# Kernel optimization log

Hardware: AMD Instinct MI355X
Metric: run time of the kernel (lower is better)

The kernel has to match this reference:

```python
import jax, jax.numpy as jnp
import numpy as np

N = 50000
E = 800000
IN, HID, OUT, MASK = 128, 96, 40, 64
THRESHOLD = 0.5


def _glorot(key, shape):
    fan_in, fan_out = shape[0], shape[1]
    lim = np.sqrt(6.0 / (fan_in + fan_out))
    return jax.random.uniform(key, shape, jnp.float32, -lim, lim)


def setup_inputs() -> dict:
    key = jax.random.key(0)
    ks = jax.random.split(key, 10)
    x = jax.random.normal(ks[0], (N, IN), jnp.float32)
    edge_index = jax.random.randint(ks[1], (2, E), 0, N, dtype=jnp.int64)
    W1 = _glorot(ks[2], (IN, HID)); b1 = jnp.zeros((HID,), jnp.float32)
    W2 = _glorot(ks[3], (HID, OUT)); b2 = jnp.zeros((OUT,), jnp.float32)
    Wm1 = _glorot(ks[4], (HID, MASK)); bm1 = jnp.zeros((MASK,), jnp.float32)
    Wm2 = _glorot(ks[5], (MASK, 1)); bm2 = jnp.zeros((1,), jnp.float32)
    return {"x": x, "edge_index": edge_index, "W1": W1, "b1": b1,
            "W2": W2, "b2": b2, "Wm1": Wm1, "bm1": bm1, "Wm2": Wm2, "bm2": bm2}


def _gcn_conv(x, src, dst, norm, W, b, n_nodes):
    # PyG GCNConv: linear transform first, then normalized scatter-add aggregation
    h = x @ W                                   # [N, out]
    msg = h[src] * norm[:, None]                # gather + scale, [E', out]
    agg = jax.ops.segment_sum(msg, dst, num_segments=n_nodes)
    return agg + b


def reference(x, edge_index, W1, b1, W2, b2, Wm1, bm1, Wm2, bm2):
    n = x.shape[0]
    # add self-loops (A + I)
    loop = jnp.arange(n, dtype=edge_index.dtype)
    src = jnp.concatenate([edge_index[0], loop])
    dst = jnp.concatenate([edge_index[1], loop])
    # symmetric normalization D^-1/2 (A+I) D^-1/2
    deg = jax.ops.segment_sum(jnp.ones_like(dst, dtype=x.dtype), dst, num_segments=n)
    dinv = jnp.where(deg > 0, jax.lax.rsqrt(deg), 0.0)
    norm = dinv[src] * dinv[dst]                # [E+N]

    h = jax.nn.relu(_gcn_conv(x, src, dst, norm, W1, b1, n))   # [N, HID]
    # dropout_p = 0.0 -> identity
    z = _gcn_conv(h, src, dst, norm, W2, b2, n)                # [N, OUT]
    logits = jax.nn.log_softmax(z, axis=1)

    prob = jax.nn.sigmoid((jax.nn.relu(h @ Wm1 + bm1) @ Wm2 + bm2)[:, 0])  # [N]
    hard = (prob > THRESHOLD).astype(prob.dtype)
    mask = prob + (hard - jax.lax.stop_gradient(prob))          # straight-through
    return (logits, prob, mask)
```

## Files before the change

### kernel.cpp

```cpp
#include <hip/hip_runtime.h>
#include <math.h>

#define IN_F  128
#define HID   96
#define OUT_F 40
#define MASKD 64

#define PBITS 8
#define PSIZE 256
#define CHUNK 2048


__global__ void k_pzero(int* __restrict__ part_total) {
    part_total[threadIdx.x] = 0;
}

__global__ void k_pcount(const int* __restrict__ dst, int* __restrict__ part_total, int e) {
    __shared__ int hist[256];
    hist[threadIdx.x] = 0;
    __syncthreads();
    int start = blockIdx.x * CHUNK, end = min(e, start + CHUNK);
    for (int i = start + threadIdx.x; i < end; i += 256)
        atomicAdd(&hist[dst[i] >> PBITS], 1);
    __syncthreads();
    int v = hist[threadIdx.x];
    if (v) atomicAdd(&part_total[threadIdx.x], v);
}

__global__ void k_pscan(const int* __restrict__ part_total, int* __restrict__ part_base,
                        int* __restrict__ part_cursor, int np) {
    __shared__ int tmp[256];
    int tid = threadIdx.x;
    int v = (tid < np) ? part_total[tid] : 0;
    tmp[tid] = v;
    __syncthreads();
    for (int d = 1; d < 256; d <<= 1) {
        int t = (tid >= d) ? tmp[tid - d] : 0;
        __syncthreads();
        tmp[tid] += t;
        __syncthreads();
    }
    int excl = tmp[tid] - v;
    if (tid < np) { part_base[tid] = excl; part_cursor[tid] = excl; }
    if (tid == 255) part_base[np] = tmp[255];
}

__global__ __launch_bounds__(256) void k_bin(const int* __restrict__ src,
                                             const int* __restrict__ dst,
                                             int* __restrict__ part_cursor,
                                             int2* __restrict__ ebuf, int e) {
    __shared__ int hist[256];
    __shared__ int cur[256];
    int tid = threadIdx.x;
    hist[tid] = 0;
    __syncthreads();
    int start = blockIdx.x * CHUNK, end = min(e, start + CHUNK);
    for (int i = start + tid; i < end; i += 256)
        atomicAdd(&hist[dst[i] >> PBITS], 1);
    __syncthreads();
    int hv = hist[tid];
    cur[tid] = hv ? atomicAdd(&part_cursor[tid], hv) : 0;
    __syncthreads();
    for (int i = start + tid; i < end; i += 256) {
        int d = dst[i];
        int pos = atomicAdd(&cur[d >> PBITS], 1);
        ebuf[pos] = make_int2(src[i], d);
    }
}

__global__ __launch_bounds__(256) void k_csr(const int2* __restrict__ ebuf,
                                             const int* __restrict__ part_base,
                                             int* __restrict__ deg, int* __restrict__ offs,
                                             float* __restrict__ dinv,
                                             int* __restrict__ csr, int n) {
    __shared__ int cnt[256];
    __shared__ int tmp[256];
    __shared__ int cur[256];
    int tid = threadIdx.x;
    int p = blockIdx.x;
    int ebase = part_base[p], eend = part_base[p + 1];
    cnt[tid] = 0;
    __syncthreads();
    for (int i = ebase + tid; i < eend; i += 256)
        atomicAdd(&cnt[ebuf[i].y & (PSIZE - 1)], 1);
    __syncthreads();
    int v = cnt[tid];
    tmp[tid] = v;
    __syncthreads();
    for (int d = 1; d < 256; d <<= 1) {
        int t = (tid >= d) ? tmp[tid - d] : 0;
        __syncthreads();
        tmp[tid] += t;
        __syncthreads();
    }
    int goff = ebase + (tmp[tid] - v);
    int node = p * PSIZE + tid;
    if (node < n) {
        deg[node] = v;
        offs[node] = goff;
        dinv[node] = rsqrtf((float)(v + 1));
    }
    cur[tid] = goff;
    __syncthreads();
    for (int i = ebase + tid; i < eend; i += 256) {
        int2 ed = ebuf[i];
        int pos = atomicAdd(&cur[ed.y & (PSIZE - 1)], 1);
        csr[pos] = ed.x;
    }
}

#define G1_ROWS 32
__global__ __launch_bounds__(192) void k_gemm1(const float* __restrict__ x,
                                               const float* __restrict__ W1,
                                               const float* __restrict__ dinv,
                                               float* __restrict__ hs, int n) {
    __shared__ float sW[IN_F * HID];
    __shared__ float sx[G1_ROWS * IN_F];
    int tid = threadIdx.x;
    int base = blockIdx.x * G1_ROWS;
    for (int i = tid; i < IN_F * HID / 4; i += 192)
        ((float4*)sW)[i] = ((const float4*)W1)[i];
    int nt = min(G1_ROWS, n - base);
    for (int i = tid; i < nt * (IN_F / 4); i += 192) {
        int r = i >> 5, kq = i & 31;
        ((float4*)sx)[r * 32 + kq] = ((const float4*)(x + (size_t)(base + r) * IN_F))[kq];
    }
    __syncthreads();

    int rt = tid / 24, ct = tid % 24;
    float acc[4][4] = {};
#pragma unroll 1
    for (int k0 = 0; k0 < IN_F; k0 += 4) {
        float4 xv[4], wv[4];
#pragma unroll
        for (int i = 0; i < 4; i++) xv[i] = *(const float4*)&sx[(rt * 4 + i) * IN_F + k0];
#pragma unroll
        for (int j = 0; j < 4; j++) wv[j] = *(const float4*)&sW[(k0 + j) * HID + ct * 4];
#pragma unroll
        for (int j = 0; j < 4; j++) {
            float4 w = wv[j];
#pragma unroll
            for (int i = 0; i < 4; i++) {
                float xs = (j == 0) ? xv[i].x : (j == 1) ? xv[i].y : (j == 2) ? xv[i].z : xv[i].w;
                acc[i][0] += xs * w.x;
                acc[i][1] += xs * w.y;
                acc[i][2] += xs * w.z;
                acc[i][3] += xs * w.w;
            }
        }
    }
#pragma unroll
    for (int i = 0; i < 4; i++) {
        int r = rt * 4 + i;
        if (r < nt) {
            int node = base + r;
            float dv = dinv[node];
            float4 o = {acc[i][0] * dv, acc[i][1] * dv, acc[i][2] * dv, acc[i][3] * dv};
            *(float4*)(hs + (size_t)node * HID + ct * 4) = o;
        }
    }
}

__global__ __launch_bounds__(256) void k_gather1(const int* __restrict__ offs,
                                                 const int* __restrict__ deg,
                                                 const int* __restrict__ csr,
                                                 const float* __restrict__ hs,
                                                 const float* __restrict__ dinv,
                                                 const float* __restrict__ b1,
                                                 float* __restrict__ h, int n) {
    int t = blockIdx.x * 256 + threadIdx.x;
    int node = t >> 5, cg = t & 31;
    if (node >= n || cg >= 24) return;
    int o = offs[node], cnt = deg[node];
    size_t col = (size_t)cg * 4;
    float4 acc = *(const float4*)(hs + (size_t)node * HID + col);
    int k = o, kend = o + cnt;
    for (; k + 3 < kend; k += 4) {
        int s0 = csr[k], s1 = csr[k + 1], s2 = csr[k + 2], s3 = csr[k + 3];
        const float4 v0 = *(const float4*)(hs + (size_t)s0 * HID + col);
        const float4 v1 = *(const float4*)(hs + (size_t)s1 * HID + col);
        const float4 v2 = *(const float4*)(hs + (size_t)s2 * HID + col);
        const float4 v3 = *(const float4*)(hs + (size_t)s3 * HID + col);
        acc.x += (v0.x + v1.x) + (v2.x + v3.x);
        acc.y += (v0.y + v1.y) + (v2.y + v3.y);
        acc.z += (v0.z + v1.z) + (v2.z + v3.z);
        acc.w += (v0.w + v1.w) + (v2.w + v3.w);
    }
    for (; k < kend; k++) {
        int s0 = csr[k];
        const float4 v0 = *(const float4*)(hs + (size_t)s0 * HID + col);
        acc.x += v0.x; acc.y += v0.y; acc.z += v0.z; acc.w += v0.w;
    }
    float dv = dinv[node];
    float4 bv = *(const float4*)(b1 + col);
    float4 o4 = {fmaxf(acc.x * dv + bv.x, 0.f), fmaxf(acc.y * dv + bv.y, 0.f),
                 fmaxf(acc.z * dv + bv.z, 0.f), fmaxf(acc.w * dv + bv.w, 0.f)};
    *(float4*)(h + (size_t)node * HID + col) = o4;
}

#define G2_ROWS 96
__global__ __launch_bounds__(256) void k_gemm2(const float* __restrict__ hbuf,
                                               const float* __restrict__ W2,
                                               const float* __restrict__ dinv,
                                               float* __restrict__ zs, int n) {
    __shared__ float sW[HID * OUT_F];
    __shared__ float sx[G2_ROWS * HID];
    int tid = threadIdx.x;
    int base = blockIdx.x * G2_ROWS;
    for (int i = tid; i < HID * OUT_F / 4; i += 256)
        ((float4*)sW)[i] = ((const float4*)W2)[i];
    int nt = min(G2_ROWS, n - base);
    for (int i = tid; i < nt * (HID / 4); i += 256) {
        int r = i / 24, kq = i % 24;
        ((float4*)sx)[r * 24 + kq] = ((const float4*)(hbuf + (size_t)(base + r) * HID))[kq];
    }
    __syncthreads();
    if (tid >= 240) return;
    int rt = tid / 10, ct = tid % 10;
    float acc[4][4] = {};
#pragma unroll 1
    for (int k0 = 0; k0 < HID; k0 += 4) {
        float4 xv[4], wv[4];
#pragma unroll
        for (int i = 0; i < 4; i++) xv[i] = *(const float4*)&sx[(rt * 4 + i) * HID + k0];
#pragma unroll
        for (int j = 0; j < 4; j++) wv[j] = *(const float4*)&sW[(k0 + j) * OUT_F + ct * 4];
#pragma unroll
        for (int j = 0; j < 4; j++) {
            float4 w = wv[j];
#pragma unroll
            for (int i = 0; i < 4; i++) {
                float xs = (j == 0) ? xv[i].x : (j == 1) ? xv[i].y : (j == 2) ? xv[i].z : xv[i].w;
                acc[i][0] += xs * w.x;
                acc[i][1] += xs * w.y;
                acc[i][2] += xs * w.z;
                acc[i][3] += xs * w.w;
            }
        }
    }
#pragma unroll
    for (int i = 0; i < 4; i++) {
        int r = rt * 4 + i;
        if (r < nt) {
            int node = base + r;
            float dv = dinv[node];
            float4 o = {acc[i][0] * dv, acc[i][1] * dv, acc[i][2] * dv, acc[i][3] * dv};
            *(float4*)(zs + (size_t)node * OUT_F + ct * 4) = o;
        }
    }
}

__global__ __launch_bounds__(256) void k_gather2(const int* __restrict__ offs,
                                                 const int* __restrict__ deg,
                                                 const int* __restrict__ csr,
                                                 const float* __restrict__ zs,
                                                 const float* __restrict__ dinv,
                                                 const float* __restrict__ b2,
                                                 float* __restrict__ out, int n) {
    int t = blockIdx.x * 256 + threadIdx.x;
    int node = t >> 4, cg = t & 15;
    if (node >= n) return;
    bool act = cg < 10;
    size_t col = (size_t)cg * 4;
    float4 acc = {0.f, 0.f, 0.f, 0.f};
    if (act) {
        acc = *(const float4*)(zs + (size_t)node * OUT_F + col);
        int o = offs[node], cnt = deg[node];
        int k = o, kend = o + cnt;
        for (; k + 3 < kend; k += 4) {
            int s0 = csr[k], s1 = csr[k + 1], s2 = csr[k + 2], s3 = csr[k + 3];
            const float4 v0 = *(const float4*)(zs + (size_t)s0 * OUT_F + col);
            const float4 v1 = *(const float4*)(zs + (size_t)s1 * OUT_F + col);
            const float4 v2 = *(const float4*)(zs + (size_t)s2 * OUT_F + col);
            const float4 v3 = *(const float4*)(zs + (size_t)s3 * OUT_F + col);
            acc.x += (v0.x + v1.x) + (v2.x + v3.x);
            acc.y += (v0.y + v1.y) + (v2.y + v3.y);
            acc.z += (v0.z + v1.z) + (v2.z + v3.z);
            acc.w += (v0.w + v1.w) + (v2.w + v3.w);
        }
        for (; k < kend; k++) {
            int s0 = csr[k];
            const float4 v0 = *(const float4*)(zs + (size_t)s0 * OUT_F + col);
            acc.x += v0.x; acc.y += v0.y; acc.z += v0.z; acc.w += v0.w;
        }
    }
    float dv = dinv[node];
    float v0 = 0.f, v1 = 0.f, v2 = 0.f, v3 = 0.f;
    if (act) {
        float4 bv = *(const float4*)(b2 + col);
        v0 = acc.x * dv + bv.x;
        v1 = acc.y * dv + bv.y;
        v2 = acc.z * dv + bv.z;
        v3 = acc.w * dv + bv.w;
    }
    float m = act ? fmaxf(fmaxf(v0, v1), fmaxf(v2, v3)) : -INFINITY;
    for (int mm = 1; mm < 16; mm <<= 1) m = fmaxf(m, __shfl_xor(m, mm, 16));
    float e = act ? (expf(v0 - m) + expf(v1 - m) + expf(v2 - m) + expf(v3 - m)) : 0.f;
    for (int mm = 1; mm < 16; mm <<= 1) e += __shfl_xor(e, mm, 16);
    float ls = logf(e);
    if (act) {
        float4 o4 = {v0 - m - ls, v1 - m - ls, v2 - m - ls, v3 - m - ls};
        *(float4*)(out + (size_t)node * OUT_F + col) = o4;
    }
}

#define MK_ROWS 64
__global__ __launch_bounds__(256) void k_mask(const float* __restrict__ h,
                                              const float* __restrict__ Wm1,
                                              const float* __restrict__ bm1,
                                              const float* __restrict__ Wm2,
                                              const float* __restrict__ bm2,
                                              float* __restrict__ prob_out,
                                              float* __restrict__ mask_out, int n) {
    __shared__ float sW[HID * MASKD];
    __shared__ float sh[MK_ROWS * HID];
    int tid = threadIdx.x;
    int base = blockIdx.x * MK_ROWS;
    for (int i = tid; i < HID * MASKD / 4; i += 256)
        ((float4*)sW)[i] = ((const float4*)Wm1)[i];
    int nt = min(MK_ROWS, n - base);
    for (int i = tid; i < nt * (HID / 4); i += 256) {
        int r = i / 24, kq = i % 24;
        ((float4*)sh)[r * 24 + kq] = ((const float4*)(h + (size_t)(base + r) * HID))[kq];
    }
    __syncthreads();
    int nt4 = tid >> 4, ct = tid & 15;
    float acc[4][4] = {};
#pragma unroll 1
    for (int k0 = 0; k0 < HID; k0 += 4) {
        float4 xv[4], wv[4];
#pragma unroll
        for (int i = 0; i < 4; i++) xv[i] = *(const float4*)&sh[(nt4 * 4 + i) * HID + k0];
#pragma unroll
        for (int j = 0; j < 4; j++) wv[j] = *(const float4*)&sW[(k0 + j) * MASKD + ct * 4];
#pragma unroll
        for (int j = 0; j < 4; j++) {
            float4 w = wv[j];
#pragma unroll
            for (int i = 0; i < 4; i++) {
                float xs = (j == 0) ? xv[i].x : (j == 1) ? xv[i].y : (j == 2) ? xv[i].z : xv[i].w;
                acc[i][0] += xs * w.x;
                acc[i][1] += xs * w.y;
                acc[i][2] += xs * w.z;
                acc[i][3] += xs * w.w;
            }
        }
    }
    float4 b1v = *(const float4*)(bm1 + ct * 4);
    float4 w2v = *(const float4*)(Wm2 + ct * 4);
    float p[4];
#pragma unroll
    for (int i = 0; i < 4; i++) {
        p[i] = fmaxf(acc[i][0] + b1v.x, 0.f) * w2v.x +
               fmaxf(acc[i][1] + b1v.y, 0.f) * w2v.y +
               fmaxf(acc[i][2] + b1v.z, 0.f) * w2v.z +
               fmaxf(acc[i][3] + b1v.w, 0.f) * w2v.w;
    }
    for (int mm = 1; mm < 16; mm <<= 1) {
#pragma unroll
        for (int i = 0; i < 4; i++) p[i] += __shfl_xor(p[i], mm, 16);
    }
    if (ct == 0) {
        float bb = bm2[0];
#pragma unroll
        for (int i = 0; i < 4; i++) {
            int r = nt4 * 4 + i;
            if (r < nt) {
                float tt = p[i] + bb;
                float pr = 1.0f / (1.0f + expf(-tt));
                prob_out[base + r] = pr;
                mask_out[base + r] = (pr > 0.5f) ? 1.0f : 0.0f;
            }
        }
    }
}

extern "C" void kernel_launch(void* const* d_in, const int* in_sizes, int n_in,
                              void* d_out, int out_size, void* d_ws, size_t ws_size,
                              hipStream_t stream) {
    const float* x   = (const float*)d_in[0];
    const int*   ei  = (const int*)d_in[1];
    const float* W1  = (const float*)d_in[2];
    const float* b1  = (const float*)d_in[3];
    const float* W2  = (const float*)d_in[4];
    const float* b2  = (const float*)d_in[5];
    const float* Wm1 = (const float*)d_in[6];
    const float* bm1 = (const float*)d_in[7];
    const float* Wm2 = (const float*)d_in[8];
    const float* bm2 = (const float*)d_in[9];

    int n = in_sizes[0] / IN_F;
    int e = in_sizes[1] / 2;
    const int* srcp = ei;
    const int* dstp = ei + e;
    int np = (n + PSIZE - 1) >> PBITS;

    float* ws   = (float*)d_ws;
    float* dinv = ws;
    float* hs   = dinv + n;
    float* h    = hs + (size_t)n * HID;
    float* zs   = h + (size_t)n * HID;
    int* deg    = (int*)(zs + (size_t)n * OUT_F);
    int* offs   = deg + n;
    int* part_total  = offs + n;
    int* part_base   = part_total + 256;
    int* part_cursor = part_base + 257;
    int* csr    = part_cursor + 256;
    int2* ebuf  = (int2*)zs;

    float* out    = (float*)d_out;
    float* logits = out;
    float* prob   = out + (size_t)n * OUT_F;
    float* mask   = prob + n;

    int ebl = (e + CHUNK - 1) / CHUNK;

    k_pzero   <<<1, 256, 0, stream>>>(part_total);
    k_pcount  <<<ebl, 256, 0, stream>>>(dstp, part_total, e);
    k_pscan   <<<1, 256, 0, stream>>>(part_total, part_base, part_cursor, np);
    k_bin     <<<ebl, 256, 0, stream>>>(srcp, dstp, part_cursor, ebuf, e);
    k_csr     <<<np, 256, 0, stream>>>(ebuf, part_base, deg, offs, dinv, csr, n);
    k_gemm1   <<<(n + G1_ROWS - 1) / G1_ROWS, 192, 0, stream>>>(x, W1, dinv, hs, n);
    k_gather1 <<<(n * 32 + 255) / 256, 256, 0, stream>>>(offs, deg, csr, hs, dinv, b1, h, n);
    k_gemm2   <<<(n + G2_ROWS - 1) / G2_ROWS, 256, 0, stream>>>(h, W2, dinv, zs, n);
    k_gather2 <<<(n * 16 + 255) / 256, 256, 0, stream>>>(offs, deg, csr, zs, dinv, b2, logits, n);
    k_mask    <<<(n + MK_ROWS - 1) / MK_ROWS, 256, 0, stream>>>(h, Wm1, bm1, Wm2, bm2, prob, mask, n);
}
```

Baseline: 281.4 us.

## Store layer-2 features in bf16 and pack edge bins into 32-bit words

Result: faster. 261.8 us (-7.0%).

```diff
diff --git a/kernel.cpp b/kernel.cpp
--- a/kernel.cpp
+++ b/kernel.cpp
@@ -10,6 +10,16 @@
 #define PSIZE 256
 #define CHUNK 2048
 
+typedef unsigned int uint;
+typedef unsigned short ushort;
+
+__device__ inline float bflo(uint u) { return __uint_as_float(u << 16); }
+__device__ inline float bfhi(uint u) { return __uint_as_float(u & 0xffff0000u); }
+__device__ inline ushort f2bf(float f) {
+    uint u = __float_as_uint(f);
+    u += 0x7fff + ((u >> 16) & 1);
+    return (ushort)(u >> 16);
+}
 
 __global__ void k_pzero(int* __restrict__ part_total) {
     part_total[threadIdx.x] = 0;
@@ -48,7 +58,7 @@
 __global__ __launch_bounds__(256) void k_bin(const int* __restrict__ src,
                                              const int* __restrict__ dst,
                                              int* __restrict__ part_cursor,
-                                             int2* __restrict__ ebuf, int e) {
+                                             uint* __restrict__ ebuf, int e) {
     __shared__ int hist[256];
     __shared__ int cur[256];
     int tid = threadIdx.x;
@@ -64,11 +74,11 @@
     for (int i = start + tid; i < end; i += 256) {
         int d = dst[i];
         int pos = atomicAdd(&cur[d >> PBITS], 1);
-        ebuf[pos] = make_int2(src[i], d);
-    }
-}
-
-__global__ __launch_bounds__(256) void k_csr(const int2* __restrict__ ebuf,
+        ebuf[pos] = (uint)src[i] | ((uint)(d & (PSIZE - 1)) << 16);
+    }
+}
+
+__global__ __launch_bounds__(256) void k_csr(const uint* __restrict__ ebuf,
                                              const int* __restrict__ part_base,
                                              int* __restrict__ deg, int* __restrict__ offs,
                                              float* __restrict__ dinv,
@@ -82,7 +92,7 @@
     cnt[tid] = 0;
     __syncthreads();
     for (int i = ebase + tid; i < eend; i += 256)
-        atomicAdd(&cnt[ebuf[i].y & (PSIZE - 1)], 1);
+        atomicAdd(&cnt[(ebuf[i] >> 16) & 255], 1);
     __syncthreads();
     int v = cnt[tid];
     tmp[tid] = v;
@@ -103,9 +113,9 @@
     cur[tid] = goff;
     __syncthreads();
     for (int i = ebase + tid; i < eend; i += 256) {
-        int2 ed = ebuf[i];
-        int pos = atomicAdd(&cur[ed.y & (PSIZE - 1)], 1);
-        csr[pos] = ed.x;
+        uint ed = ebuf[i];
+        int pos = atomicAdd(&cur[(ed >> 16) & 255], 1);
+        csr[pos] = (int)(ed & 0xffffu);
     }
 }
 
@@ -202,7 +212,7 @@
 __global__ __launch_bounds__(256) void k_gemm2(const float* __restrict__ hbuf,
                                                const float* __restrict__ W2,
                                                const float* __restrict__ dinv,
-                                               float* __restrict__ zs, int n) {
+                                               ushort* __restrict__ zs_b, int n) {
     __shared__ float sW[HID * OUT_F];
     __shared__ float sx[G2_ROWS * HID];
     int tid = threadIdx.x;
@@ -244,8 +254,9 @@
         if (r < nt) {
             int node = base + r;
             float dv = dinv[node];
-            float4 o = {acc[i][0] * dv, acc[i][1] * dv, acc[i][2] * dv, acc[i][3] * dv};
-            *(float4*)(zs + (size_t)node * OUT_F + ct * 4) = o;
+            ushort4 o = {f2bf(acc[i][0] * dv), f2bf(acc[i][1] * dv),
+                         f2bf(acc[i][2] * dv), f2bf(acc[i][3] * dv)};
+            *(ushort4*)(zs_b + (size_t)node * OUT_F + ct * 4) = o;
         }
     }
 }
@@ -253,54 +264,76 @@
 __global__ __launch_bounds__(256) void k_gather2(const int* __restrict__ offs,
                                                  const int* __restrict__ deg,
                                                  const int* __restrict__ csr,
-                                                 const float* __restrict__ zs,
+                                                 const ushort* __restrict__ zs_b,
                                                  const float* __restrict__ dinv,
                                                  const float* __restrict__ b2,
                                                  float* __restrict__ out, int n) {
     int t = blockIdx.x * 256 + threadIdx.x;
-    int node = t >> 4, cg = t & 15;
+    int node = t >> 3, cg = t & 7;
     if (node >= n) return;
-    bool act = cg < 10;
-    size_t col = (size_t)cg * 4;
-    float4 acc = {0.f, 0.f, 0.f, 0.f};
+    bool act = cg < 5;
+    const uint4* zsr = (const uint4*)zs_b;
+    float acc[8] = {};
     if (act) {
-        acc = *(const float4*)(zs + (size_t)node * OUT_F + col);
+        uint4 sv = zsr[(size_t)node * 5 + cg];
+        acc[0] = bflo(sv.x); acc[1] = bfhi(sv.x);
+        acc[2] = bflo(sv.y); acc[3] = bfhi(sv.y);
+        acc[4] = bflo(sv.z); acc[5] = bfhi(sv.z);
+        acc[6] = bflo(sv.w); acc[7] = bfhi(sv.w);
         int o = offs[node], cnt = deg[node];
         int k = o, kend = o + cnt;
         for (; k + 3 < kend; k += 4) {
             int s0 = csr[k], s1 = csr[k + 1], s2 = csr[k + 2], s3 = csr[k + 3];
-            const float4 v0 = *(const float4*)(zs + (size_t)s0 * OUT_F + col);
-            const float4 v1 = *(const float4*)(zs + (size_t)s1 * OUT_F + col);
-            const float4 v2 = *(const float4*)(zs + (size_t)s2 * OUT_F + col);
-            const float4 v3 = *(const float4*)(zs + (size_t)s3 * OUT_F + col);
-            acc.x += (v0.x + v1.x) + (v2.x + v3.x);
-            acc.y += (v0.y + v1.y) + (v2.y + v3.y);
-            acc.z += (v0.z + v1.z) + (v2.z + v3.z);
-            acc.w += (v0.w + v1.w) + (v2.w + v3.w);
+            uint4 v0 = zsr[(size_t)s0 * 5 + cg];
+            uint4 v1 = zsr[(size_t)s1 * 5 + cg];
+            uint4 v2 = zsr[(size_t)s2 * 5 + cg];
+            uint4 v3 = zsr[(size_t)s3 * 5 + cg];
+            acc[0] += (bflo(v0.x) + bflo(v1.x)) + (bflo(v2.x) + bflo(v3.x));
+            acc[1] += (bfhi(v0.x) + bfhi(v1.x)) + (bfhi(v2.x) + bfhi(v3.x));
+            acc[2] += (bflo(v0.y) + bflo(v1.y)) + (bflo(v2.y) + bflo(v3.y));
+            acc[3] += (bfhi(v0.y) + bfhi(v1.y)) + (bfhi(v2.y) + bfhi(v3.y));
+            acc[4] += (bflo(v0.z) + bflo(v1.z)) + (bflo(v2.z) + bflo(v3.z));
+            acc[5] += (bfhi(v0.z) + bfhi(v1.z)) + (bfhi(v2.z) + bfhi(v3.z));
+            acc[6] += (bflo(v0.w) + bflo(v1.w)) + (bflo(v2.w) + bflo(v3.w));
+            acc[7] += (bfhi(v0.w) + bfhi(v1.w)) + (bfhi(v2.w) + bfhi(v3.w));
         }
         for (; k < kend; k++) {
-            int s0 = csr[k];
-            const float4 v0 = *(const float4*)(zs + (size_t)s0 * OUT_F + col);
-            acc.x += v0.x; acc.y += v0.y; acc.z += v0.z; acc.w += v0.w;
+            uint4 v0 = zsr[(size_t)csr[k] * 5 + cg];
+            acc[0] += bflo(v0.x); acc[1] += bfhi(v0.x);
+            acc[2] += bflo(v0.y); acc[3] += bfhi(v0.y);
+            acc[4] += bflo(v0.z); acc[5] += bfhi(v0.z);
+            acc[6] += bflo(v0.w); acc[7] += bfhi(v0.w);
         }
     }
     float dv = dinv[node];
-    float v0 = 0.f, v1 = 0.f, v2 = 0.f, v3 = 0.f;
+    float v[8];
+    float m = -INFINITY;
     if (act) {
-        float4 bv = *(const float4*)(b2 + col);
-        v0 = acc.x * dv + bv.x;
-        v1 = acc.y * dv + bv.y;
-        v2 = acc.z * dv + bv.z;
-        v3 = acc.w * dv + bv.w;
-    }
-    float m = act ? fmaxf(fmaxf(v0, v1), fmaxf(v2, v3)) : -INFINITY;
-    for (int mm = 1; mm < 16; mm <<= 1) m = fmaxf(m, __shfl_xor(m, mm, 16));
-    float e = act ? (expf(v0 - m) + expf(v1 - m) + expf(v2 - m) + expf(v3 - m)) : 0.f;
-    for (int mm = 1; mm < 16; mm <<= 1) e += __shfl_xor(e, mm, 16);
+        int col = cg * 8;
+        float4 ba = *(const float4*)(b2 + col);
+        float4 bb = *(const float4*)(b2 + col + 4);
+        v[0] = acc[0] * dv + ba.x; v[1] = acc[1] * dv + ba.y;
+        v[2] = acc[2] * dv + ba.z; v[3] = acc[3] * dv + ba.w;
+        v[4] = acc[4] * dv + bb.x; v[5] = acc[5] * dv + bb.y;
+        v[6] = acc[6] * dv + bb.z; v[7] = acc[7] * dv + bb.w;
+#pragma unroll
+        for (int i = 0; i < 8; i++) m = fmaxf(m, v[i]);
+    }
+    for (int mm = 1; mm < 8; mm <<= 1) m = fmaxf(m, __shfl_xor(m, mm, 8));
+    float e = 0.f;
+    if (act) {
+#pragma unroll
+        for (int i = 0; i < 8; i++) e += expf(v[i] - m);
+    }
+    for (int mm = 1; mm < 8; mm <<= 1) e += __shfl_xor(e, mm, 8);
     float ls = logf(e);
     if (act) {
-        float4 o4 = {v0 - m - ls, v1 - m - ls, v2 - m - ls, v3 - m - ls};
-        *(float4*)(out + (size_t)node * OUT_F + col) = o4;
+        int col = cg * 8;
+        float4 oa = {v[0] - m - ls, v[1] - m - ls, v[2] - m - ls, v[3] - m - ls};
+        float4 ob = {v[4] - m - ls, v[5] - m - ls, v[6] - m - ls, v[7] - m - ls};
+        float* op = out + (size_t)node * OUT_F + col;
+        *(float4*)op = oa;
+        *(float4*)(op + 4) = ob;
     }
 }
 
@@ -395,18 +428,18 @@
     const int* dstp = ei + e;
     int np = (n + PSIZE - 1) >> PBITS;
 
-    float* ws   = (float*)d_ws;
-    float* dinv = ws;
-    float* hs   = dinv + n;
-    float* h    = hs + (size_t)n * HID;
-    float* zs   = h + (size_t)n * HID;
-    int* deg    = (int*)(zs + (size_t)n * OUT_F);
-    int* offs   = deg + n;
-    int* part_total  = offs + n;
-    int* part_base   = part_total + 256;
-    int* part_cursor = part_base + 257;
-    int* csr    = part_cursor + 256;
-    int2* ebuf  = (int2*)zs;
+    char* wsb = (char*)d_ws;
+    float* dinv = (float*)wsb;            wsb += (((size_t)n * 4) + 255) & ~(size_t)255;
+    float* hs = (float*)wsb;              wsb += (((size_t)n * HID * 4) + 255) & ~(size_t)255;
+    float* h = (float*)wsb;               wsb += (((size_t)n * HID * 4) + 255) & ~(size_t)255;
+    ushort* zs_b = (ushort*)wsb;          wsb += (((size_t)n * OUT_F * 2) + 255) & ~(size_t)255;
+    int* deg = (int*)wsb;                 wsb += (((size_t)n * 4) + 255) & ~(size_t)255;
+    int* offs = (int*)wsb;                wsb += (((size_t)n * 4) + 255) & ~(size_t)255;
+    int* part_total = (int*)wsb;          wsb += 1024;
+    int* part_base = (int*)wsb;           wsb += 2048;
+    int* part_cursor = (int*)wsb;         wsb += 1024;
+    int* csr = (int*)wsb;                 wsb += (((size_t)e * 4) + 255) & ~(size_t)255;
+    uint* ebuf = (uint*)wsb;              wsb += (((size_t)e * 4) + 255) & ~(size_t)255;
 
     float* out    = (float*)d_out;
     float* logits = out;
@@ -422,7 +455,7 @@
     k_csr     <<<np, 256, 0, stream>>>(ebuf, part_base, deg, offs, dinv, csr, n);
     k_gemm1   <<<(n + G1_ROWS - 1) / G1_ROWS, 192, 0, stream>>>(x, W1, dinv, hs, n);
     k_gather1 <<<(n * 32 + 255) / 256, 256, 0, stream>>>(offs, deg, csr, hs, dinv, b1, h, n);
-    k_gemm2   <<<(n + G2_ROWS - 1) / G2_ROWS, 256, 0, stream>>>(h, W2, dinv, zs, n);
-    k_gather2 <<<(n * 16 + 255) / 256, 256, 0, stream>>>(offs, deg, csr, zs, dinv, b2, logits, n);
+    k_gemm2   <<<(n + G2_ROWS - 1) / G2_ROWS, 256, 0, stream>>>(h, W2, dinv, zs_b, n);
+    k_gather2 <<<(n * 8 + 255) / 256, 256, 0, stream>>>(offs, deg, csr, zs_b, dinv, b2, logits, n);
     k_mask    <<<(n + MK_ROWS - 1) / MK_ROWS, 256, 0, stream>>>(h, Wm1, bm1, Wm2, bm2, prob, mask, n);
 }
```
